# Optimization experiments

Hardware: AMD Instinct MI355X
Metric: run time of the kernel (lower is better)

## Reference

```python
import jax, jax.numpy as jnp
import numpy as np

HEAD_DIM = 128
BAND_BITS = (5, 4, 4, 3)
N_BANDS = len(BAND_BITS)
BAND = HEAD_DIM // N_BANDS  # 32
FP16_MAX = 65504.0


def _hadamard(n):
    H = np.array([[1.0]], dtype=np.float32)
    while H.shape[0] < n:
        H = np.block([[H, H], [H, -H]])
    return H


def _mobius_perm(n):
    # Mobius function mu(i) for i = 1..n via sieve
    mu = np.ones(n + 1, dtype=np.int64)
    is_prime = np.ones(n + 1, dtype=bool)
    for p in range(2, n + 1):
        if is_prime[p]:
            is_prime[2 * p::p] = False
            mu[p::p] *= -1
            sq = p * p
            if sq <= n:
                mu[sq::sq] = 0
    # stable reorder of the 0..n-1 coordinates by descending mu(i+1)
    perm = np.argsort(-mu[1:n + 1], kind='stable').astype(np.int32)
    inv = np.argsort(perm).astype(np.int32)
    return perm, inv

_H = jnp.asarray(_hadamard(HEAD_DIM))            # [128,128], symmetric, H@H = 128*I
_PERM, _INV_PERM = (jnp.asarray(p) for p in _mobius_perm(HEAD_DIM))


def _banded_quant_dequant(z):
    # z: [N, HEAD_DIM] in WHT+Mobius space. Per-row, per-band symmetric quantization.
    zb = z.reshape(-1, N_BANDS, BAND)                       # [N, 4, 32]
    qmax = jnp.asarray([2 ** (b - 1) - 1 for b in BAND_BITS], jnp.float32)  # [4]
    amax = jnp.max(jnp.abs(zb), axis=-1)                    # [N, 4]
    scale = jnp.where(amax > 0, amax / qmax, 1.0)           # [N, 4]
    q = jnp.clip(jnp.round(zb / scale[..., None]), -qmax[:, None], qmax[:, None])
    return (q * scale[..., None]).reshape(-1, HEAD_DIM)


def setup_inputs() -> dict:
    key = jax.random.key(0)
    k1, k2 = jax.random.split(key)
    x = jax.random.normal(k1, (2, 512, 5120), dtype=jnp.float32)
    W = jax.random.normal(k2, (5120, 5120), dtype=jnp.float32) * 0.02
    b = jnp.zeros((5120,), dtype=jnp.float32)
    return {"x": x, "W": W, "b": b}


def reference(x, W, b):
    # cache-miss path: linear projection (result = cross_attn proj of T5 context)
    y = jnp.einsum('bld,ed->ble', x, W) + b                 # [B, L, 5120]
    orig_shape = y.shape
    yf = y.reshape(-1, HEAD_DIM)                            # [B*L*n_heads, 128]
    # put(): WHT -> Mobius reorder -> banded quantize
    z = yf @ _H                                             # unnormalized WHT
    z = z[:, _PERM]
    z = _banded_quant_dequant(z)
    # get(): un-reorder -> inverse WHT (WHT then /head_dim) -> clamp/nan_to_num
    z = z[:, _INV_PERM]
    r = (z @ _H) / HEAD_DIM
    r = jnp.clip(r, -FP16_MAX, FP16_MAX)
    r = jnp.nan_to_num(r, nan=0.0)
    return r.reshape(orig_shape)
```

## Files before the change

kernel.cpp:

```cpp
#include <hip/hip_runtime.h>
#include <math.h>

#define HEAD 128
typedef _Float16 f16;
typedef _Float16 f16x8 __attribute__((ext_vector_type(8)));
typedef _Float16 f16x4 __attribute__((ext_vector_type(4)));
typedef float f32x4 __attribute__((ext_vector_type(4)));

constexpr int mu_of(int n) {
  int m = n, cnt = 0;
  for (int p = 2; p * p <= m; ++p) {
    if (m % p == 0) {
      m /= p; ++cnt;
      if (m % p == 0) return 0;
    }
  }
  if (m > 1) ++cnt;
  return (cnt & 1) ? -1 : 1;
}
constexpr int key_of(int idx) {
  int mu = mu_of(idx + 1);
  return mu == 1 ? 0 : (mu == 0 ? 1 : 2);
}
struct Tbl {
  int band[HEAD];
  float qm[HEAD];
};
constexpr Tbl make_tbl() {
  Tbl t{};
  constexpr float qv[4] = {15.f, 7.f, 7.f, 3.f};
  for (int p = 0; p < HEAD; ++p) {
    int kp = key_of(p);
    int rank = 0;
    for (int j = 0; j < HEAD; ++j) {
      int kj = key_of(j);
      if (kj < kp || (kj == kp && j < p)) ++rank;
    }
    t.band[p] = rank >> 5;
    t.qm[p] = qv[rank >> 5];
  }
  return t;
}
__constant__ Tbl g_tbl = make_tbl();

__global__ __launch_bounds__(256) void split64(const float* __restrict__ s,
                                               f16* __restrict__ h,
                                               f16* __restrict__ l, int n4) {
  int i = blockIdx.x * blockDim.x + threadIdx.x;
  if (i >= n4) return;
  float4 v = ((const float4*)s)[i];
  v.x *= 64.f; v.y *= 64.f; v.z *= 64.f; v.w *= 64.f;
  f16 hx = (f16)v.x, hy = (f16)v.y, hz = (f16)v.z, hw = (f16)v.w;
  f16 lx = (f16)(v.x - (float)hx);
  f16 ly = (f16)(v.y - (float)hy);
  f16 lz = (f16)(v.z - (float)hz);
  f16 lw = (f16)(v.w - (float)hw);
  f16x4 hv = {hx, hy, hz, hw};
  f16x4 lv = {lx, ly, lz, lw};
  *(f16x4*)(h + 4 * (size_t)i) = hv;
  *(f16x4*)(l + 4 * (size_t)i) = lv;
}

__device__ __forceinline__ void dma16(const f16* g, f16* l) {
  __builtin_amdgcn_global_load_lds(
      (const __attribute__((address_space(1))) unsigned int*)g,
      (__attribute__((address_space(3))) unsigned int*)l, 16, 0, 0);
}

__global__ __launch_bounds__(64) void gemm_f16split(
    const f16* __restrict__ Ah, const f16* __restrict__ Al,
    const f16* __restrict__ Bh, const f16* __restrict__ Bl,
    const float* __restrict__ bias, float* __restrict__ C,
    int M, int N, int K) {
  __shared__ f16 sAh[64 * 32];
  __shared__ f16 sAl[64 * 32];
  __shared__ f16 sBh[64 * 32];
  __shared__ f16 sBl[64 * 32];

  const int lane = threadIdx.x;
  const int m0 = blockIdx.x * 64;
  const int n0 = blockIdx.y * 64;

  const int srow = lane >> 2;
  const int scol = (lane & 3) * 8;
  const f16* gAh = Ah + (size_t)(m0 + srow) * K + scol;
  const f16* gAl = Al + (size_t)(m0 + srow) * K + scol;
  const f16* gBh = Bh + (size_t)(n0 + srow) * K + scol;
  const f16* gBl = Bl + (size_t)(n0 + srow) * K + scol;
  const size_t rstep = (size_t)16 * K;

  f32x4 acc[4][4];
#pragma unroll
  for (int i = 0; i < 4; ++i)
#pragma unroll
    for (int j = 0; j < 4; ++j) acc[i][j] = (f32x4){0.f, 0.f, 0.f, 0.f};

#pragma unroll
  for (int j = 0; j < 4; ++j) {
    dma16(gAh + j * rstep, &sAh[j * 512]);
    dma16(gAl + j * rstep, &sAl[j * 512]);
    dma16(gBh + j * rstep, &sBh[j * 512]);
    dma16(gBl + j * rstep, &sBl[j * 512]);
  }

  const int frow = lane & 15;
  const int kq = lane >> 4;
  const int fbase = frow * 32 + kq * 8;

  for (int k0 = 0; k0 < K; k0 += 32) {
    __syncthreads();
    f16x8 ah[4], al[4], bh[4], bl[4];
#pragma unroll
    for (int s = 0; s < 4; ++s) {
      ah[s] = *(const f16x8*)&sAh[s * 512 + fbase];
      al[s] = *(const f16x8*)&sAl[s * 512 + fbase];
      bh[s] = *(const f16x8*)&sBh[s * 512 + fbase];
      bl[s] = *(const f16x8*)&sBl[s * 512 + fbase];
    }
    __syncthreads();
    if (k0 + 32 < K) {
      const int kn = k0 + 32;
#pragma unroll
      for (int j = 0; j < 4; ++j) {
        dma16(gAh + kn + j * rstep, &sAh[j * 512]);
        dma16(gAl + kn + j * rstep, &sAl[j * 512]);
        dma16(gBh + kn + j * rstep, &sBh[j * 512]);
        dma16(gBl + kn + j * rstep, &sBl[j * 512]);
      }
    }
#pragma unroll
    for (int i = 0; i < 4; ++i)
#pragma unroll
      for (int j = 0; j < 4; ++j) {
        acc[i][j] = __builtin_amdgcn_mfma_f32_16x16x32_f16(ah[i], bh[j], acc[i][j], 0, 0, 0);
        acc[i][j] = __builtin_amdgcn_mfma_f32_16x16x32_f16(al[i], bh[j], acc[i][j], 0, 0, 0);
        acc[i][j] = __builtin_amdgcn_mfma_f32_16x16x32_f16(ah[i], bl[j], acc[i][j], 0, 0, 0);
      }
  }

  const float inv = 1.f / 4096.f;
#pragma unroll
  for (int j = 0; j < 4; ++j) {
    const int col = n0 + j * 16 + frow;
    const float bv = bias[col];
#pragma unroll
    for (int i = 0; i < 4; ++i) {
#pragma unroll
      for (int r = 0; r < 4; ++r) {
        const int row = m0 + i * 16 + kq * 4 + r;
        C[(size_t)row * N + col] = acc[i][j][r] * inv + bv;
      }
    }
  }
}

#define BM 128
#define BN 64
#define BKK 8
#define TM 8
#define TN 4

__global__ __launch_bounds__(256) void sgemm_nt(
    const float* __restrict__ A, const float* __restrict__ B,
    const float* __restrict__ bias, float* __restrict__ C,
    int M, int N, int K) {
  __shared__ float As[BKK][BM];
  __shared__ float Bs[BKK][BN];

  const int tid = threadIdx.x;
  const int tn = tid & 15;
  const int tm = tid >> 4;
  const int bx = blockIdx.x;
  const int by = blockIdx.y;

  const float* Ab = A + (size_t)by * BM * K;
  const float* Bb = B + (size_t)bx * BN * K;

  const int ar = tid >> 1;
  const int ak = (tid & 1) * 4;

  float acc[TM][TN];
#pragma unroll
  for (int i = 0; i < TM; ++i)
#pragma unroll
    for (int j = 0; j < TN; ++j) acc[i][j] = 0.f;

  for (int k0 = 0; k0 < K; k0 += BKK) {
    float4 av = *(const float4*)(Ab + (size_t)ar * K + k0 + ak);
    float4 bv = make_float4(0.f, 0.f, 0.f, 0.f);
    if (tid < 128) bv = *(const float4*)(Bb + (size_t)ar * K + k0 + ak);

    __syncthreads();
    As[ak + 0][ar] = av.x;
    As[ak + 1][ar] = av.y;
    As[ak + 2][ar] = av.z;
    As[ak + 3][ar] = av.w;
    if (tid < 128) {
      Bs[ak + 0][ar] = bv.x;
      Bs[ak + 1][ar] = bv.y;
      Bs[ak + 2][ar] = bv.z;
      Bs[ak + 3][ar] = bv.w;
    }
    __syncthreads();

#pragma unroll
    for (int kk = 0; kk < BKK; ++kk) {
      float a[TM], b[TN];
#pragma unroll
      for (int i = 0; i < TM; ++i) a[i] = As[kk][tm * TM + i];
#pragma unroll
      for (int j = 0; j < TN; ++j) b[j] = Bs[kk][tn * TN + j];
#pragma unroll
      for (int i = 0; i < TM; ++i)
#pragma unroll
        for (int j = 0; j < TN; ++j) acc[i][j] += a[i] * b[j];
    }
  }

  const int row0 = by * BM + tm * TM;
  const int col0 = bx * BN + tn * TN;
  float bj[TN];
#pragma unroll
  for (int j = 0; j < TN; ++j) bj[j] = bias[col0 + j];
#pragma unroll
  for (int i = 0; i < TM; ++i) {
    float4 v = make_float4(acc[i][0] + bj[0], acc[i][1] + bj[1],
                           acc[i][2] + bj[2], acc[i][3] + bj[3]);
    *(float4*)(C + (size_t)(row0 + i) * N + col0) = v;
  }
}

__device__ inline void fwht2(float& e0, float& e1, int lane) {
  float a = e0 + e1;
  float b = e0 - e1;
  e0 = a;
  e1 = b;
#pragma unroll
  for (int s = 1; s <= 32; s <<= 1) {
    float p0 = __shfl_xor(e0, s);
    float p1 = __shfl_xor(e1, s);
    bool up = (lane & s) != 0;
    e0 = up ? (p0 - e0) : (e0 + p0);
    e1 = up ? (p1 - e1) : (e1 + p1);
  }
}

__global__ __launch_bounds__(256) void hadq(const float* __restrict__ Y,
                                            float* __restrict__ O, int nrows) {
  const int lane = threadIdx.x & 63;
  const int wave = (blockIdx.x * (blockDim.x >> 6)) + (threadIdx.x >> 6);
  const int nwaves = gridDim.x * (blockDim.x >> 6);

  const int b0 = g_tbl.band[lane];
  const int b1 = g_tbl.band[lane + 64];
  const float qm0 = g_tbl.qm[lane];
  const float qm1 = g_tbl.qm[lane + 64];

  for (int row = wave; row < nrows; row += nwaves) {
    const float* y = Y + (size_t)row * HEAD;
    float e0 = y[lane];
    float e1 = y[lane + 64];

    fwht2(e0, e1, lane);

    float f0 = fabsf(e0), f1 = fabsf(e1);
    float ab0 = fmaxf(b0 == 0 ? f0 : 0.f, b1 == 0 ? f1 : 0.f);
    float ab1 = fmaxf(b0 == 1 ? f0 : 0.f, b1 == 1 ? f1 : 0.f);
    float ab2 = fmaxf(b0 == 2 ? f0 : 0.f, b1 == 2 ? f1 : 0.f);
    float ab3 = fmaxf(b0 == 3 ? f0 : 0.f, b1 == 3 ? f1 : 0.f);
#pragma unroll
    for (int s = 32; s >= 1; s >>= 1) {
      ab0 = fmaxf(ab0, __shfl_xor(ab0, s));
      ab1 = fmaxf(ab1, __shfl_xor(ab1, s));
      ab2 = fmaxf(ab2, __shfl_xor(ab2, s));
      ab3 = fmaxf(ab3, __shfl_xor(ab3, s));
    }
    float am0 = b0 == 0 ? ab0 : (b0 == 1 ? ab1 : (b0 == 2 ? ab2 : ab3));
    float am1 = b1 == 0 ? ab0 : (b1 == 1 ? ab1 : (b1 == 2 ? ab2 : ab3));

    float s0 = am0 > 0.f ? am0 / qm0 : 1.0f;
    float s1 = am1 > 0.f ? am1 / qm1 : 1.0f;

    float q0 = fminf(fmaxf(rintf(e0 / s0), -qm0), qm0);
    float q1 = fminf(fmaxf(rintf(e1 / s1), -qm1), qm1);
    e0 = q0 * s0;
    e1 = q1 * s1;

    fwht2(e0, e1, lane);
    float r0 = e0 * 0.0078125f;
    float r1 = e1 * 0.0078125f;
    if (r0 != r0) r0 = 0.f;
    if (r1 != r1) r1 = 0.f;
    r0 = fminf(fmaxf(r0, -65504.f), 65504.f);
    r1 = fminf(fmaxf(r1, -65504.f), 65504.f);

    float* o = O + (size_t)row * HEAD;
    o[lane] = r0;
    o[lane + 64] = r1;
  }
}

extern "C" void kernel_launch(void* const* d_in, const int* in_sizes, int n_in,
                              void* d_out, int out_size, void* d_ws, size_t ws_size,
                              hipStream_t stream) {
  const float* x = (const float*)d_in[0];
  const float* W = (const float*)d_in[1];
  const float* b = (const float*)d_in[2];
  float* out = (float*)d_out;

  const int N = in_sizes[2];
  const int K = N;
  const int M = in_sizes[0] / K;

  const size_t MK = (size_t)M * K;
  const size_t NK = (size_t)N * K;
  const size_t need = (MK + NK) * 2 * sizeof(f16);

  if (ws_size >= need) {
    f16* xh = (f16*)d_ws;
    f16* xl = xh + MK;
    f16* wh = xl + MK;
    f16* wl = wh + NK;

    const int n4x = (int)(MK / 4);
    const int n4w = (int)(NK / 4);
    split64<<<(n4x + 255) / 256, 256, 0, stream>>>(x, xh, xl, n4x);
    split64<<<(n4w + 255) / 256, 256, 0, stream>>>(W, wh, wl, n4w);

    dim3 grid(M / 64, N / 64);
    gemm_f16split<<<grid, 64, 0, stream>>>(xh, xl, wh, wl, b, out, M, N, K);
  } else {
    dim3 grid(N / BN, M / BM);
    sgemm_nt<<<grid, 256, 0, stream>>>(x, W, b, out, M, N, K);
  }

  const int nrows = out_size / HEAD;
  hadq<<<512, 256, 0, stream>>>(out, out, nrows);
}
```

Baseline: 493.7 us.

## Double-buffer LDS in split-f16 GEMM with explicit waitcnt instead of barriers

Turns the single LDS stage of the split-f16 MFMA GEMM into a two-stage ring. The next-next tile's async global-to-LDS loads are issued right after the current fragments are read. The two __syncthreads are replaced with hand-written s_waitcnt vmcnt/lgkmcnt encodings, which is valid because the block is a single wavefront. The goal is to hide global load latency behind the MFMAs. It doubles LDS use and relies on hardcoded waitcnt bit encodings (vmcnt 16) matching the number of outstanding DMA loads, which is fragile on this architecture.

```diff
diff --git a/kernel.cpp b/kernel.cpp
--- a/kernel.cpp
+++ b/kernel.cpp
@@ -6,6 +6,10 @@
 typedef _Float16 f16x8 __attribute__((ext_vector_type(8)));
 typedef _Float16 f16x4 __attribute__((ext_vector_type(4)));
 typedef float f32x4 __attribute__((ext_vector_type(4)));
+
+#define WC_VM16 0x4F70
+#define WC_VM0  0x0F70
+#define WC_LGKM0 0xC07F
 
 constexpr int mu_of(int n) {
   int m = n, cnt = 0;
@@ -72,10 +76,8 @@
     const f16* __restrict__ Bh, const f16* __restrict__ Bl,
     const float* __restrict__ bias, float* __restrict__ C,
     int M, int N, int K) {
-  __shared__ f16 sAh[64 * 32];
-  __shared__ f16 sAl[64 * 32];
-  __shared__ f16 sBh[64 * 32];
-  __shared__ f16 sBl[64 * 32];
+  __shared__ f16 sA[2][2][64 * 32];
+  __shared__ f16 sB[2][2][64 * 32];
 
   const int lane = threadIdx.x;
   const int m0 = blockIdx.x * 64;
@@ -95,39 +97,46 @@
 #pragma unroll
     for (int j = 0; j < 4; ++j) acc[i][j] = (f32x4){0.f, 0.f, 0.f, 0.f};
 
-#pragma unroll
-  for (int j = 0; j < 4; ++j) {
-    dma16(gAh + j * rstep, &sAh[j * 512]);
-    dma16(gAl + j * rstep, &sAl[j * 512]);
-    dma16(gBh + j * rstep, &sBh[j * 512]);
-    dma16(gBl + j * rstep, &sBl[j * 512]);
-  }
+#define STAGE(buf, kofs)                                   \
+  do {                                                     \
+    _Pragma("unroll") for (int j = 0; j < 4; ++j) {        \
+      dma16(gAh + (kofs) + j * rstep, &sA[buf][0][j * 512]); \
+      dma16(gAl + (kofs) + j * rstep, &sA[buf][1][j * 512]); \
+      dma16(gBh + (kofs) + j * rstep, &sB[buf][0][j * 512]); \
+      dma16(gBl + (kofs) + j * rstep, &sB[buf][1][j * 512]); \
+    }                                                      \
+  } while (0)
+
+  STAGE(0, 0);
+  STAGE(1, 32);
 
   const int frow = lane & 15;
   const int kq = lane >> 4;
   const int fbase = frow * 32 + kq * 8;
 
-  for (int k0 = 0; k0 < K; k0 += 32) {
-    __syncthreads();
+  const int nIter = K / 32;
+  for (int it = 0; it < nIter; ++it) {
+    const int buf = it & 1;
+    if (it + 1 == nIter)
+      __builtin_amdgcn_s_waitcnt(WC_VM0);
+    else
+      __builtin_amdgcn_s_waitcnt(WC_VM16);
+    __asm__ volatile("" ::: "memory");
+
     f16x8 ah[4], al[4], bh[4], bl[4];
 #pragma unroll
     for (int s = 0; s < 4; ++s) {
-      ah[s] = *(const f16x8*)&sAh[s * 512 + fbase];
-      al[s] = *(const f16x8*)&sAl[s * 512 + fbase];
-      bh[s] = *(const f16x8*)&sBh[s * 512 + fbase];
-      bl[s] = *(const f16x8*)&sBl[s * 512 + fbase];
-    }
-    __syncthreads();
-    if (k0 + 32 < K) {
-      const int kn = k0 + 32;
-#pragma unroll
-      for (int j = 0; j < 4; ++j) {
-        dma16(gAh + kn + j * rstep, &sAh[j * 512]);
-        dma16(gAl + kn + j * rstep, &sAl[j * 512]);
-        dma16(gBh + kn + j * rstep, &sBh[j * 512]);
-        dma16(gBl + kn + j * rstep, &sBl[j * 512]);
-      }
-    }
+      ah[s] = *(const f16x8*)&sA[buf][0][s * 512 + fbase];
+      al[s] = *(const f16x8*)&sA[buf][1][s * 512 + fbase];
+      bh[s] = *(const f16x8*)&sB[buf][0][s * 512 + fbase];
+      bl[s] = *(const f16x8*)&sB[buf][1][s * 512 + fbase];
+    }
+    __asm__ volatile("" ::: "memory");
+    __builtin_amdgcn_s_waitcnt(WC_LGKM0);
+    __asm__ volatile("" ::: "memory");
+
+    if (it + 2 < nIter) STAGE(buf, (it + 2) * 32);
+
 #pragma unroll
     for (int i = 0; i < 4; ++i)
 #pragma unroll
@@ -152,6 +161,7 @@
       }
     }
   }
+#undef STAGE
 }
 
 #define BM 128
```

Result: slower. 554.9 us (+12.4%).

## Split K four ways with atomic accumulation and conflict-free LDS fragment layout

Applied to the files above, without the earlier changes.

The f16-split GEMM now splits the K dimension four ways across grid.z, giving four times as many single-wave blocks to fill the GPU. Partial sums are combined with atomic adds into an output that a new kernel pre-fills with the bias. The LDS staging order is remapped so that each lane's fragment read is contiguous, which should avoid bank conflicts, and the fp32-to-f16 hi/lo split kernel now handles 8 elements per thread. In exchange there is extra atomic traffic to global memory, an extra bias-fill pass, and a summation order that is no longer deterministic.

```diff
diff --git a/kernel.cpp b/kernel.cpp
--- a/kernel.cpp
+++ b/kernel.cpp
@@ -4,7 +4,6 @@
 #define HEAD 128
 typedef _Float16 f16;
 typedef _Float16 f16x8 __attribute__((ext_vector_type(8)));
-typedef _Float16 f16x4 __attribute__((ext_vector_type(4)));
 typedef float f32x4 __attribute__((ext_vector_type(4)));
 
 constexpr int mu_of(int n) {
@@ -43,22 +42,33 @@
 }
 __constant__ Tbl g_tbl = make_tbl();
 
-__global__ __launch_bounds__(256) void split64(const float* __restrict__ s,
-                                               f16* __restrict__ h,
-                                               f16* __restrict__ l, int n4) {
+__global__ __launch_bounds__(256) void bias_init(const float* __restrict__ b,
+                                                 float* __restrict__ C,
+                                                 int n4col, int total4) {
   int i = blockIdx.x * blockDim.x + threadIdx.x;
-  if (i >= n4) return;
-  float4 v = ((const float4*)s)[i];
-  v.x *= 64.f; v.y *= 64.f; v.z *= 64.f; v.w *= 64.f;
-  f16 hx = (f16)v.x, hy = (f16)v.y, hz = (f16)v.z, hw = (f16)v.w;
-  f16 lx = (f16)(v.x - (float)hx);
-  f16 ly = (f16)(v.y - (float)hy);
-  f16 lz = (f16)(v.z - (float)hz);
-  f16 lw = (f16)(v.w - (float)hw);
-  f16x4 hv = {hx, hy, hz, hw};
-  f16x4 lv = {lx, ly, lz, lw};
-  *(f16x4*)(h + 4 * (size_t)i) = hv;
-  *(f16x4*)(l + 4 * (size_t)i) = lv;
+  if (i >= total4) return;
+  int c4 = i % n4col;
+  ((float4*)C)[i] = ((const float4*)b)[c4];
+}
+
+__global__ __launch_bounds__(256) void split8(const float* __restrict__ s,
+                                              f16* __restrict__ h,
+                                              f16* __restrict__ l, int n8) {
+  int i = blockIdx.x * blockDim.x + threadIdx.x;
+  if (i >= n8) return;
+  const float4* p = (const float4*)s + 2 * (size_t)i;
+  float4 a = p[0], c = p[1];
+  float v[8] = {a.x, a.y, a.z, a.w, c.x, c.y, c.z, c.w};
+  f16x8 hv, lv;
+#pragma unroll
+  for (int j = 0; j < 8; ++j) {
+    float sv = v[j] * 64.f;
+    f16 hj = (f16)sv;
+    hv[j] = hj;
+    lv[j] = (f16)(sv - (float)hj);
+  }
+  ((f16x8*)h)[i] = hv;
+  ((f16x8*)l)[i] = lv;
 }
 
 __device__ __forceinline__ void dma16(const f16* g, f16* l) {
@@ -67,26 +77,23 @@
       (__attribute__((address_space(3))) unsigned int*)l, 16, 0, 0);
 }
 
-__global__ __launch_bounds__(64) void gemm_f16split(
+__global__ __launch_bounds__(64) void gemm_f16split_sk(
     const f16* __restrict__ Ah, const f16* __restrict__ Al,
     const f16* __restrict__ Bh, const f16* __restrict__ Bl,
-    const float* __restrict__ bias, float* __restrict__ C,
-    int M, int N, int K) {
-  __shared__ f16 sAh[64 * 32];
-  __shared__ f16 sAl[64 * 32];
-  __shared__ f16 sBh[64 * 32];
-  __shared__ f16 sBl[64 * 32];
+    float* __restrict__ C, int M, int N, int K, int KC) {
+  __shared__ f16 sAh[2048], sAl[2048], sBh[2048], sBl[2048];
 
   const int lane = threadIdx.x;
   const int m0 = blockIdx.x * 64;
   const int n0 = blockIdx.y * 64;
-
-  const int srow = lane >> 2;
-  const int scol = (lane & 3) * 8;
-  const f16* gAh = Ah + (size_t)(m0 + srow) * K + scol;
-  const f16* gAl = Al + (size_t)(m0 + srow) * K + scol;
-  const f16* gBh = Bh + (size_t)(n0 + srow) * K + scol;
-  const f16* gBl = Bl + (size_t)(n0 + srow) * K + scol;
+  const int kbeg = blockIdx.z * KC;
+
+  const int srow = lane & 15;
+  const int scol = (lane >> 4) * 8;
+  const f16* gAh = Ah + (size_t)(m0 + srow) * K + kbeg + scol;
+  const f16* gAl = Al + (size_t)(m0 + srow) * K + kbeg + scol;
+  const f16* gBh = Bh + (size_t)(n0 + srow) * K + kbeg + scol;
+  const f16* gBl = Bl + (size_t)(n0 + srow) * K + kbeg + scol;
   const size_t rstep = (size_t)16 * K;
 
   f32x4 acc[4][4];
@@ -95,19 +102,24 @@
 #pragma unroll
     for (int j = 0; j < 4; ++j) acc[i][j] = (f32x4){0.f, 0.f, 0.f, 0.f};
 
-#pragma unroll
-  for (int j = 0; j < 4; ++j) {
-    dma16(gAh + j * rstep, &sAh[j * 512]);
-    dma16(gAl + j * rstep, &sAl[j * 512]);
-    dma16(gBh + j * rstep, &sBh[j * 512]);
-    dma16(gBl + j * rstep, &sBl[j * 512]);
-  }
+#define STAGE(kofs)                                  \
+  do {                                               \
+    _Pragma("unroll") for (int j = 0; j < 4; ++j) {  \
+      dma16(gAh + (kofs) + j * rstep, &sAh[j * 512]); \
+      dma16(gAl + (kofs) + j * rstep, &sAl[j * 512]); \
+      dma16(gBh + (kofs) + j * rstep, &sBh[j * 512]); \
+      dma16(gBl + (kofs) + j * rstep, &sBl[j * 512]); \
+    }                                                \
+  } while (0)
+
+  STAGE(0);
 
   const int frow = lane & 15;
   const int kq = lane >> 4;
-  const int fbase = frow * 32 + kq * 8;
-
-  for (int k0 = 0; k0 < K; k0 += 32) {
+  const int fbase = frow * 8 + kq * 128;
+
+  const int nIter = KC / 32;
+  for (int it = 0; it < nIter; ++it) {
     __syncthreads();
     f16x8 ah[4], al[4], bh[4], bl[4];
 #pragma unroll
@@ -118,16 +130,8 @@
       bl[s] = *(const f16x8*)&sBl[s * 512 + fbase];
     }
     __syncthreads();
-    if (k0 + 32 < K) {
-      const int kn = k0 + 32;
-#pragma unroll
-      for (int j = 0; j < 4; ++j) {
-        dma16(gAh + kn + j * rstep, &sAh[j * 512]);
-        dma16(gAl + kn + j * rstep, &sAl[j * 512]);
-        dma16(gBh + kn + j * rstep, &sBh[j * 512]);
-        dma16(gBl + kn + j * rstep, &sBl[j * 512]);
-      }
-    }
+    if (it + 1 < nIter) STAGE((it + 1) * 32);
+
 #pragma unroll
     for (int i = 0; i < 4; ++i)
 #pragma unroll
@@ -142,16 +146,16 @@
 #pragma unroll
   for (int j = 0; j < 4; ++j) {
     const int col = n0 + j * 16 + frow;
-    const float bv = bias[col];
 #pragma unroll
     for (int i = 0; i < 4; ++i) {
 #pragma unroll
       for (int r = 0; r < 4; ++r) {
         const int row = m0 + i * 16 + kq * 4 + r;
-        C[(size_t)row * N + col] = acc[i][j][r] * inv + bv;
+        unsafeAtomicAdd(&C[(size_t)row * N + col], acc[i][j][r] * inv);
       }
     }
   }
+#undef STAGE
 }
 
 #define BM 128
@@ -322,13 +326,17 @@
     f16* wh = xl + MK;
     f16* wl = wh + NK;
 
-    const int n4x = (int)(MK / 4);
-    const int n4w = (int)(NK / 4);
-    split64<<<(n4x + 255) / 256, 256, 0, stream>>>(x, xh, xl, n4x);
-    split64<<<(n4w + 255) / 256, 256, 0, stream>>>(W, wh, wl, n4w);
-
-    dim3 grid(M / 64, N / 64);
-    gemm_f16split<<<grid, 64, 0, stream>>>(xh, xl, wh, wl, b, out, M, N, K);
+    const int n8x = (int)(MK / 8);
+    const int n8w = (int)(NK / 8);
+    split8<<<(n8x + 255) / 256, 256, 0, stream>>>(x, xh, xl, n8x);
+    split8<<<(n8w + 255) / 256, 256, 0, stream>>>(W, wh, wl, n8w);
+
+    const int total4 = M * N / 4;
+    bias_init<<<(total4 + 255) / 256, 256, 0, stream>>>(b, out, N / 4, total4);
+
+    const int SK = 4;
+    dim3 grid(M / 64, N / 64, SK);
+    gemm_f16split_sk<<<grid, 64, 0, stream>>>(xh, xl, wh, wl, out, M, N, K, K / SK);
   } else {
     dim3 grid(N / BN, M / BM);
     sgemm_nt<<<grid, 256, 0, stream>>>(x, W, b, out, M, N, K);
```

Measured after the change: 633.2 us. +28.3%, slower.

## Merge split kernels and double K-tile depth in split-f16 MFMA GEMM

Applied to the files above, without the earlier changes.

Fuses the two fp32-to-f16 hi/lo split launches into one grid-stride kernel that processes 8 elements per thread. The GEMM now stages 64 K-columns per barrier pair instead of 32, with a changed LDS layout (row = lane&15, column group = lane>>4). Each iteration issues twice as many MFMAs per sync, aiming to amortize barrier and DMA latency. The cost is more LDS and more register pressure from the doubled fragment arrays.

```diff
diff --git a/kernel.cpp b/kernel.cpp
--- a/kernel.cpp
+++ b/kernel.cpp
@@ -4,7 +4,6 @@
 #define HEAD 128
 typedef _Float16 f16;
 typedef _Float16 f16x8 __attribute__((ext_vector_type(8)));
-typedef _Float16 f16x4 __attribute__((ext_vector_type(4)));
 typedef float f32x4 __attribute__((ext_vector_type(4)));
 
 constexpr int mu_of(int n) {
@@ -43,22 +42,36 @@
 }
 __constant__ Tbl g_tbl = make_tbl();
 
-__global__ __launch_bounds__(256) void split64(const float* __restrict__ s,
-                                               f16* __restrict__ h,
-                                               f16* __restrict__ l, int n4) {
-  int i = blockIdx.x * blockDim.x + threadIdx.x;
-  if (i >= n4) return;
-  float4 v = ((const float4*)s)[i];
-  v.x *= 64.f; v.y *= 64.f; v.z *= 64.f; v.w *= 64.f;
-  f16 hx = (f16)v.x, hy = (f16)v.y, hz = (f16)v.z, hw = (f16)v.w;
-  f16 lx = (f16)(v.x - (float)hx);
-  f16 ly = (f16)(v.y - (float)hy);
-  f16 lz = (f16)(v.z - (float)hz);
-  f16 lw = (f16)(v.w - (float)hw);
-  f16x4 hv = {hx, hy, hz, hw};
-  f16x4 lv = {lx, ly, lz, lw};
-  *(f16x4*)(h + 4 * (size_t)i) = hv;
-  *(f16x4*)(l + 4 * (size_t)i) = lv;
+__global__ __launch_bounds__(256) void split_all(
+    const float* __restrict__ x, const float* __restrict__ W,
+    f16* __restrict__ xh, f16* __restrict__ xl,
+    f16* __restrict__ wh, f16* __restrict__ wl,
+    long n8x, long n8tot) {
+  long i = blockIdx.x * (long)blockDim.x + threadIdx.x;
+  long stride = (long)gridDim.x * blockDim.x;
+  for (; i < n8tot; i += stride) {
+    const float* s;
+    f16 *h, *l;
+    long j;
+    if (i < n8x) {
+      s = x; h = xh; l = xl; j = i;
+    } else {
+      s = W; h = wh; l = wl; j = i - n8x;
+    }
+    const float4* p = (const float4*)s + 2 * j;
+    float4 a = p[0], c = p[1];
+    float v[8] = {a.x, a.y, a.z, a.w, c.x, c.y, c.z, c.w};
+    f16x8 hv, lv;
+#pragma unroll
+    for (int t = 0; t < 8; ++t) {
+      float sv = v[t] * 64.f;
+      f16 ht = (f16)sv;
+      hv[t] = ht;
+      lv[t] = (f16)(sv - (float)ht);
+    }
+    ((f16x8*)h)[j] = hv;
+    ((f16x8*)l)[j] = lv;
+  }
 }
 
 __device__ __forceinline__ void dma16(const f16* g, f16* l) {
@@ -72,17 +85,14 @@
     const f16* __restrict__ Bh, const f16* __restrict__ Bl,
     const float* __restrict__ bias, float* __restrict__ C,
     int M, int N, int K) {
-  __shared__ f16 sAh[64 * 32];
-  __shared__ f16 sAl[64 * 32];
-  __shared__ f16 sBh[64 * 32];
-  __shared__ f16 sBl[64 * 32];
+  __shared__ f16 sAh[4096], sAl[4096], sBh[4096], sBl[4096];
 
   const int lane = threadIdx.x;
   const int m0 = blockIdx.x * 64;
   const int n0 = blockIdx.y * 64;
 
-  const int srow = lane >> 2;
-  const int scol = (lane & 3) * 8;
+  const int srow = lane & 15;
+  const int scol = (lane >> 4) * 8;
   const f16* gAh = Ah + (size_t)(m0 + srow) * K + scol;
   const f16* gAl = Al + (size_t)(m0 + srow) * K + scol;
   const f16* gBh = Bh + (size_t)(n0 + srow) * K + scol;
@@ -95,47 +105,53 @@
 #pragma unroll
     for (int j = 0; j < 4; ++j) acc[i][j] = (f32x4){0.f, 0.f, 0.f, 0.f};
 
-#pragma unroll
-  for (int j = 0; j < 4; ++j) {
-    dma16(gAh + j * rstep, &sAh[j * 512]);
-    dma16(gAl + j * rstep, &sAl[j * 512]);
-    dma16(gBh + j * rstep, &sBh[j * 512]);
-    dma16(gBl + j * rstep, &sBl[j * 512]);
-  }
+#define STAGE(kofs)                                                    \
+  do {                                                                 \
+    _Pragma("unroll") for (int s = 0; s < 4; ++s) {                    \
+      _Pragma("unroll") for (int h = 0; h < 2; ++h) {                  \
+        const size_t go = (kofs) + s * rstep + h * 32;                 \
+        const int lo = s * 1024 + h * 512;                             \
+        dma16(gAh + go, &sAh[lo]);                                     \
+        dma16(gAl + go, &sAl[lo]);                                     \
+        dma16(gBh + go, &sBh[lo]);                                     \
+        dma16(gBl + go, &sBl[lo]);                                     \
+      }                                                                \
+    }                                                                  \
+  } while (0)
+
+  STAGE(0);
 
   const int frow = lane & 15;
   const int kq = lane >> 4;
-  const int fbase = frow * 32 + kq * 8;
-
-  for (int k0 = 0; k0 < K; k0 += 32) {
+  const int fbase = frow * 8 + kq * 128;
+
+  const int nIter = K / 64;
+  for (int it = 0; it < nIter; ++it) {
     __syncthreads();
-    f16x8 ah[4], al[4], bh[4], bl[4];
-#pragma unroll
-    for (int s = 0; s < 4; ++s) {
-      ah[s] = *(const f16x8*)&sAh[s * 512 + fbase];
-      al[s] = *(const f16x8*)&sAl[s * 512 + fbase];
-      bh[s] = *(const f16x8*)&sBh[s * 512 + fbase];
-      bl[s] = *(const f16x8*)&sBl[s * 512 + fbase];
-    }
+    f16x8 ah[2][4], al[2][4], bh[2][4], bl[2][4];
+#pragma unroll
+    for (int st = 0; st < 2; ++st)
+#pragma unroll
+      for (int s = 0; s < 4; ++s) {
+        const int o = s * 1024 + st * 512 + fbase;
+        ah[st][s] = *(const f16x8*)&sAh[o];
+        al[st][s] = *(const f16x8*)&sAl[o];
+        bh[st][s] = *(const f16x8*)&sBh[o];
+        bl[st][s] = *(const f16x8*)&sBl[o];
+      }
     __syncthreads();
-    if (k0 + 32 < K) {
-      const int kn = k0 + 32;
-#pragma unroll
-      for (int j = 0; j < 4; ++j) {
-        dma16(gAh + kn + j * rstep, &sAh[j * 512]);
-        dma16(gAl + kn + j * rstep, &sAl[j * 512]);
-        dma16(gBh + kn + j * rstep, &sBh[j * 512]);
-        dma16(gBl + kn + j * rstep, &sBl[j * 512]);
-      }
-    }
-#pragma unroll
-    for (int i = 0; i < 4; ++i)
-#pragma unroll
-      for (int j = 0; j < 4; ++j) {
-        acc[i][j] = __builtin_amdgcn_mfma_f32_16x16x32_f16(ah[i], bh[j], acc[i][j], 0, 0, 0);
-        acc[i][j] = __builtin_amdgcn_mfma_f32_16x16x32_f16(al[i], bh[j], acc[i][j], 0, 0, 0);
-        acc[i][j] = __builtin_amdgcn_mfma_f32_16x16x32_f16(ah[i], bl[j], acc[i][j], 0, 0, 0);
-      }
+    if (it + 1 < nIter) STAGE((size_t)(it + 1) * 64);
+
+#pragma unroll
+    for (int st = 0; st < 2; ++st)
+#pragma unroll
+      for (int i = 0; i < 4; ++i)
+#pragma unroll
+        for (int j = 0; j < 4; ++j) {
+          acc[i][j] = __builtin_amdgcn_mfma_f32_16x16x32_f16(ah[st][i], bh[st][j], acc[i][j], 0, 0, 0);
+          acc[i][j] = __builtin_amdgcn_mfma_f32_16x16x32_f16(al[st][i], bh[st][j], acc[i][j], 0, 0, 0);
+          acc[i][j] = __builtin_amdgcn_mfma_f32_16x16x32_f16(ah[st][i], bl[st][j], acc[i][j], 0, 0, 0);
+        }
   }
 
   const float inv = 1.f / 4096.f;
@@ -152,6 +168,7 @@
       }
     }
   }
+#undef STAGE
 }
 
 #define BM 128
@@ -322,10 +339,9 @@
     f16* wh = xl + MK;
     f16* wl = wh + NK;
 
-    const int n4x = (int)(MK / 4);
-    const int n4w = (int)(NK / 4);
-    split64<<<(n4x + 255) / 256, 256, 0, stream>>>(x, xh, xl, n4x);
-    split64<<<(n4w + 255) / 256, 256, 0, stream>>>(W, wh, wl, n4w);
+    const long n8x = (long)(MK / 8);
+    const long n8tot = (long)((MK + NK) / 8);
+    split_all<<<4096, 256, 0, stream>>>(x, W, xh, xl, wh, wl, n8x, n8tot);
 
     dim3 grid(M / 64, N / 64);
     gemm_f16split<<<grid, 64, 0, stream>>>(xh, xl, wh, wl, b, out, M, N, K);
```

New measurement: 741.9 us. 50.3% more time.
